# Kernel optimization log

Measured on AMD Instinct MI355X. Metric: run time of the kernel, lower is better.

The kernel has to match this reference:

```python
import jax, jax.numpy as jnp
import numpy as np

B, CIN, COUT, K, H, W = 16, 256, 256, 3, 64, 64
COND = 512


def setup_inputs() -> dict:
    key = jax.random.key(0)
    ks = jax.random.split(key, 10)
    X = jax.random.normal(ks[0], (B, CIN, H, W), dtype=jnp.float32)
    cond_v = jax.random.normal(ks[1], (B, COND), dtype=jnp.float32)
    # conv weight [O, I, kh, kw]
    conv_w = jax.random.normal(ks[2], (COUT, CIN, K, K), dtype=jnp.float32) / np.sqrt(CIN * K * K)
    w0 = jax.random.normal(ks[3], (COND, COND), dtype=jnp.float32) / np.sqrt(COND)
    b0 = jnp.zeros((COND,), dtype=jnp.float32)
    w1 = jax.random.normal(ks[4], (COND, COND), dtype=jnp.float32) / np.sqrt(COND)
    b1 = jnp.zeros((COND,), dtype=jnp.float32)
    w_out = jax.random.normal(ks[5], (CIN, COND), dtype=jnp.float32) / np.sqrt(COND)
    b_out = jnp.zeros((CIN,), dtype=jnp.float32)
    return {"X": X, "cond_v": cond_v, "conv_w": conv_w,
            "w0": w0, "b0": b0, "w1": w1, "b1": b1,
            "w_out": w_out, "b_out": b_out}


def reference(X, cond_v, conv_w, w0, b0, w1, b1, w_out, b_out):
    # proj_cond MLP: (Linear+SiLU) x depth, final Linear -> in_channels
    h = jax.nn.silu(cond_v @ w0.T + b0)
    h = jax.nn.silu(h @ w1.T + b1)
    scale = h @ w_out.T + b_out + 1.0          # [B, I]
    # modulate: bw[b,o,i,kh,kw] = w[o,i,kh,kw] * scale[b,i]
    bw = conv_w[None] * scale[:, None, :, None, None]
    # demodulate across (i, kh, kw)
    demod = jax.lax.rsqrt(jnp.sum(bw * bw, axis=(2, 3, 4)) + 1e-8)  # [B, O]
    bw = bw * demod[:, :, None, None, None]
    b, o, i, kh, kw = bw.shape
    # per-sample conv via grouped conv: x -> [1, B*I, H, W], w -> [B*O, I, kh, kw]
    x = X.reshape(1, b * i, X.shape[2], X.shape[3])
    w = bw.reshape(b * o, i, kh, kw)
    out = jax.lax.conv_general_dilated(
        x, w, window_strides=(1, 1), padding="SAME",
        feature_group_count=b,
        dimension_numbers=("NCHW", "OIHW", "NCHW"))
    return out.reshape(b, o, out.shape[2], out.shape[3])
```

## Files before the change

### kernel.cpp

```cpp
#include <hip/hip_runtime.h>
#include <hip/hip_bf16.h>
#include <cstdint>

#define NB 16
#define CI 256
#define CO 256
#define HH 64
#define WW 64
#define CC 512
#define HP 66
#define WP 66

typedef short short8 __attribute__((ext_vector_type(8)));
typedef float floatx4 __attribute__((ext_vector_type(4)));
typedef unsigned int uintx4 __attribute__((ext_vector_type(4)));

__device__ __forceinline__ void g2lds16(const void* g, void* l) {
  __builtin_amdgcn_global_load_lds((const __attribute__((address_space(1))) void*)g,
                                   (__attribute__((address_space(3))) void*)l, 16, 0, 0);
}

#define ASM_VMCNT0() do { asm volatile("s_waitcnt vmcnt(0)" ::: "memory"); \
                          __builtin_amdgcn_sched_barrier(0); } while (0)
#define ASM_VMCNT2() do { asm volatile("s_waitcnt vmcnt(2)" ::: "memory"); \
                          __builtin_amdgcn_sched_barrier(0); } while (0)
#define RAW_BAR() do { __builtin_amdgcn_sched_barrier(0);  \
                       __builtin_amdgcn_s_barrier();       \
                       __builtin_amdgcn_sched_barrier(0); } while (0)

__global__ void k_zero_halo(__hip_bfloat16* __restrict__ Xs) {
  int gid = blockIdx.x * 256 + threadIdx.x;
  int job = gid >> 5;
  int unit = gid & 31;
  int b = job / 260;
  int p = job % 260;
  if (b >= NB) return;
  int hp, wp;
  if (p < 66)       { hp = 0;       wp = p; }
  else if (p < 132) { hp = 65;      wp = p - 66; }
  else if (p < 196) { hp = p - 131; wp = 0; }
  else              { hp = p - 195; wp = 65; }
  uintx4 z = {0u, 0u, 0u, 0u};
  *reinterpret_cast<uintx4*>(Xs + ((((size_t)b * HP + hp) * WP + wp) * CI + unit * 8)) = z;
}

template<int KD, int N, bool SILU, bool PLUSONE, int BJ>
__global__ void k_mlp(const float* __restrict__ in, const float* __restrict__ w,
                      const float* __restrict__ bias, float* __restrict__ out) {
  __shared__ float4 sin4[KD / 4];
  const int nb = N / BJ;
  int b = blockIdx.x / nb;
  int j = (blockIdx.x % nb) * BJ + threadIdx.x;
  const float4* in4 = reinterpret_cast<const float4*>(in + (size_t)b * KD);
  for (int k = threadIdx.x; k < KD / 4; k += BJ) sin4[k] = in4[k];
  __syncthreads();
  float acc = bias[j];
  const float4* wr = reinterpret_cast<const float4*>(w + (size_t)j * KD);
#pragma unroll 8
  for (int kk = 0; kk < KD / 4; ++kk) {
    float4 wv = wr[kk];
    float4 sv = sin4[kk];
    acc += wv.x * sv.x + wv.y * sv.y + wv.z * sv.z + wv.w * sv.w;
  }
  if (SILU) acc = acc / (1.0f + __expf(-acc));
  if (PLUSONE) acc += 1.0f;
  out[(size_t)b * N + j] = acc;
}

__global__ void k_repack(const float* __restrict__ cw, __hip_bfloat16* __restrict__ Wt,
                         float* __restrict__ wsq) {
  int gid = blockIdx.x * 256 + threadIdx.x;
  if (gid >= CO * CI) return;
  const float* p = cw + (size_t)gid * 9;
  float s = 0.0f;
#pragma unroll
  for (int t = 0; t < 9; ++t) {
    float v = p[t];
    s += v * v;
    Wt[(size_t)t * CO * CI + gid] = __float2bfloat16(v);
  }
  wsq[gid] = s;
}

__global__ void k_demod(const float* __restrict__ wsq, const float* __restrict__ scale,
                        float* __restrict__ demod) {
  __shared__ float s2[CI];
  int b = blockIdx.x;
  int o = threadIdx.x;
  float sv = scale[b * CI + o];
  s2[o] = sv * sv;
  __syncthreads();
  float acc = 0.0f;
  const float4* wr = reinterpret_cast<const float4*>(wsq + (size_t)o * CI);
  const float4* s4 = reinterpret_cast<const float4*>(s2);
#pragma unroll 8
  for (int i = 0; i < CI / 4; ++i) {
    float4 wv = wr[i];
    float4 sq = s4[i];
    acc += wv.x * sq.x + wv.y * sq.y + wv.z * sq.z + wv.w * sq.w;
  }
  demod[b * CO + o] = rsqrtf(acc + 1e-8f);
}

__global__ void k_scalex(const float* __restrict__ X, const float* __restrict__ scale,
                         __hip_bfloat16* __restrict__ Xs) {
  __shared__ float tile[64][68];
  __shared__ float ssc[64];
  int bid = blockIdx.x;
  int b = bid >> 8;
  int rem = bid & 255;
  int h = rem >> 2;
  int i0 = (rem & 3) * 64;
  int t = threadIdx.x;
  if (t < 64) ssc[t] = scale[b * CI + i0 + t];
  const float* src = X + (((size_t)b * CI + i0) * HH + h) * WW;
  int ii_base = t >> 4;
  int w4 = (t & 15) * 4;
#pragma unroll
  for (int r2 = 0; r2 < 4; ++r2) {
    int ii = r2 * 16 + ii_base;
    *reinterpret_cast<float4*>(&tile[ii][w4]) =
        *reinterpret_cast<const float4*>(src + (size_t)ii * HH * WW + w4);
  }
  __syncthreads();
  int u = t & 7;
  int wl = t >> 3;
#pragma unroll
  for (int iter = 0; iter < 2; ++iter) {
    int w2 = wl + iter * 32;
    union { unsigned short us[8]; uintx4 v; } pk;
#pragma unroll
    for (int j = 0; j < 8; ++j) {
      int ii = u * 8 + j;
      float v = tile[ii][w2] * ssc[ii];
      __hip_bfloat16 hb = __float2bfloat16(v);
      pk.us[j] = *reinterpret_cast<unsigned short*>(&hb);
    }
    *reinterpret_cast<uintx4*>(Xs + ((((size_t)b * HP + (h + 1)) * WP + (w2 + 1)) * CI + i0 + u * 8)) = pk.v;
  }
}

__global__ __launch_bounds__(512, 4)
void k_conv(const __hip_bfloat16* __restrict__ Xs, const __hip_bfloat16* __restrict__ Wt,
            const float* __restrict__ demod, float* __restrict__ out) {
  __shared__ __align__(16) char lds[33792 + 2 * 16384];
  char* sX  = lds;
  char* sA0 = lds + 33792;

  int bid = blockIdx.x;
  int b = bid >> 6;
  int rem = bid & 63;
  int ht = rem >> 1;
  int ob = rem & 1;
  int h0 = ht * 2;
  int o0 = ob * 128;

  int tid = threadIdx.x;
  int wv = tid >> 6;
  int lane = tid & 63;
  int lhi = lane >> 4;
  int llo = lane & 15;
  int wo = wv >> 2;
  int wq = wv & 3;
  int r = wq >> 1;
  int c0 = (wq & 1) * 32;

  floatx4 acc[4][2];
#pragma unroll
  for (int m = 0; m < 4; ++m)
#pragma unroll
    for (int n = 0; n < 2; ++n) acc[m][n] = (floatx4){0.f, 0.f, 0.f, 0.f};

  int row_a[4], ra7[4];
#pragma unroll
  for (int m = 0; m < 4; ++m) { row_a[m] = wo * 64 + m * 16 + llo; ra7[m] = row_a[m] & 7; }

  const __hip_bfloat16* xs_img = Xs + (size_t)b * HP * WP * CI;

  for (int ic = 0; ic < 4; ++ic) {
    for (int j = wv; j < 33; j += 8) {
      int u = j * 64 + lane;
      int row = u >> 3;
      int slot = lane & 7;
      int lr = row / 66;
      int wp = row - lr * 66;
      int isel = ic * 64 + ((slot ^ (row & 7)) << 3);
      const __hip_bfloat16* src = xs_img + (((size_t)(h0 + lr) * WP + wp) * CI + isel);
      g2lds16(src, sX + j * 1024);
    }
    {
      const __hip_bfloat16* wbase = Wt + (size_t)o0 * CI + ic * 64;
#pragma unroll
      for (int jj = 0; jj < 2; ++jj) {
        int j = wv + jj * 8;
        int row = j * 8 + (lane >> 3);
        int slot = lane & 7;
        int isel = (slot ^ (row & 7)) << 3;
        g2lds16(wbase + (size_t)row * CI + isel, sA0 + j * 1024);
      }
    }
    ASM_VMCNT0();
    RAW_BAR();

    for (int t = 0; t < 9; ++t) {
      char* sA = sA0 + (t & 1) * 16384;
      if (t < 8) {
        const __hip_bfloat16* wbase = Wt + (size_t)(t + 1) * CO * CI + (size_t)o0 * CI + ic * 64;
        char* dst = sA0 + ((t + 1) & 1) * 16384;
#pragma unroll
        for (int jj = 0; jj < 2; ++jj) {
          int j = wv + jj * 8;
          int row = j * 8 + (lane >> 3);
          int slot = lane & 7;
          int isel = (slot ^ (row & 7)) << 3;
          g2lds16(wbase + (size_t)row * CI + isel, dst + j * 1024);
        }
        ASM_VMCNT2();
      } else {
        ASM_VMCNT0();
      }
      RAW_BAR();

      int kh = t / 3;
      int kw = t - kh * 3;
#pragma unroll
      for (int k32 = 0; k32 < 2; ++k32) {
        short8 af[4], bq[2];
#pragma unroll
        for (int m = 0; m < 4; ++m) {
          int addr = row_a[m] * 128 + (((k32 * 4 + lhi) ^ ra7[m]) << 4);
          af[m] = *reinterpret_cast<const short8*>(sA + addr);
        }
#pragma unroll
        for (int n = 0; n < 2; ++n) {
          int tr = (r + kh) * 66 + c0 + n * 16 + llo + kw;
          int addr = tr * 128 + (((k32 * 4 + lhi) ^ (tr & 7)) << 4);
          bq[n] = *reinterpret_cast<const short8*>(sX + addr);
        }
#pragma unroll
        for (int m = 0; m < 4; ++m)
#pragma unroll
          for (int n = 0; n < 2; ++n)
            acc[m][n] = __builtin_amdgcn_mfma_f32_16x16x32_bf16(af[m], bq[n], acc[m][n], 0, 0, 0);
      }
      RAW_BAR();
    }
  }

  const float* dmrow = demod + b * CO + o0 + wo * 64;
  float* obase = out + (((size_t)b * CO + o0 + wo * 64) * HH + (h0 + r)) * WW;
#pragma unroll
  for (int m = 0; m < 4; ++m) {
#pragma unroll
    for (int j = 0; j < 4; ++j) {
      int o_off = m * 16 + lhi * 4 + j;
      float dm = dmrow[o_off];
#pragma unroll
      for (int n = 0; n < 2; ++n) {
        int w = c0 + n * 16 + llo;
        obase[(size_t)o_off * HH * WW + w] = acc[m][n][j] * dm;
      }
    }
  }
}

extern "C" void kernel_launch(void* const* d_in, const int* in_sizes, int n_in,
                              void* d_out, int out_size, void* d_ws, size_t ws_size,
                              hipStream_t stream) {
  const float* X      = (const float*)d_in[0];
  const float* cond_v = (const float*)d_in[1];
  const float* conv_w = (const float*)d_in[2];
  const float* w0     = (const float*)d_in[3];
  const float* b0     = (const float*)d_in[4];
  const float* w1     = (const float*)d_in[5];
  const float* b1     = (const float*)d_in[6];
  const float* w_out  = (const float*)d_in[7];
  const float* b_out  = (const float*)d_in[8];
  float* out = (float*)d_out;

  char* ws = (char*)d_ws;
  const size_t XS_BYTES  = (size_t)NB * HP * WP * CI * 2;
  const size_t WT_BYTES  = (size_t)9 * CO * CI * 2;
  const size_t WSQ_BYTES = (size_t)CO * CI * 4;
  __hip_bfloat16* Xs = (__hip_bfloat16*)ws;
  __hip_bfloat16* Wt = (__hip_bfloat16*)(ws + XS_BYTES);
  float* wsq   = (float*)(ws + XS_BYTES + WT_BYTES);
  float* h0b   = (float*)(ws + XS_BYTES + WT_BYTES + WSQ_BYTES);
  float* h1b   = h0b + NB * CC;
  float* scale = h1b + NB * CC;
  float* demod = scale + NB * CI;

  k_zero_halo<<<520, 256, 0, stream>>>(Xs);
  k_repack<<<(CO * CI) / 256, 256, 0, stream>>>(conv_w, Wt, wsq);
  k_mlp<CC, CC, true, false, 128><<<NB * (CC / 128), 128, 0, stream>>>(cond_v, w0, b0, h0b);
  k_mlp<CC, CC, true, false, 128><<<NB * (CC / 128), 128, 0, stream>>>(h0b, w1, b1, h1b);
  k_mlp<CC, CI, false, true, 128><<<NB * (CI / 128), 128, 0, stream>>>(h1b, w_out, b_out, scale);
  k_demod<<<NB, CO, 0, stream>>>(wsq, scale, demod);
  k_scalex<<<NB * 64 * 4, 256, 0, stream>>>(X, scale, Xs);
  k_conv<<<NB * 32 * 2, 512, 0, stream>>>(Xs, Wt, demod, out);
}
```

Before: 139.2 us.

## Enlarge conv tile to all output channels, fuse halo zeroing, swizzle transpose tile

The conv kernel now gives each workgroup all 256 output channels and 4 output rows, so the input halo tile is loaded once per workgroup instead of twice. Each wave accumulates 4x8 MFMA tiles, and a remapped block index spreads work across XCDs. Halo zeroing moves into the scale/transpose kernel, removing one launch, and that kernel's LDS transpose tile gets an XOR swizzle to cut bank conflicts. The trade-off is far higher LDS and register use per block (occupancy bound drops from 4 to 2) and only 256 workgroups in the grid, which may underfill the GPU.

```diff
diff --git a/kernel.cpp b/kernel.cpp
--- a/kernel.cpp
+++ b/kernel.cpp
@@ -22,27 +22,11 @@
 
 #define ASM_VMCNT0() do { asm volatile("s_waitcnt vmcnt(0)" ::: "memory"); \
                           __builtin_amdgcn_sched_barrier(0); } while (0)
-#define ASM_VMCNT2() do { asm volatile("s_waitcnt vmcnt(2)" ::: "memory"); \
+#define ASM_VMCNT4() do { asm volatile("s_waitcnt vmcnt(4)" ::: "memory"); \
                           __builtin_amdgcn_sched_barrier(0); } while (0)
 #define RAW_BAR() do { __builtin_amdgcn_sched_barrier(0);  \
                        __builtin_amdgcn_s_barrier();       \
                        __builtin_amdgcn_sched_barrier(0); } while (0)
-
-__global__ void k_zero_halo(__hip_bfloat16* __restrict__ Xs) {
-  int gid = blockIdx.x * 256 + threadIdx.x;
-  int job = gid >> 5;
-  int unit = gid & 31;
-  int b = job / 260;
-  int p = job % 260;
-  if (b >= NB) return;
-  int hp, wp;
-  if (p < 66)       { hp = 0;       wp = p; }
-  else if (p < 132) { hp = 65;      wp = p - 66; }
-  else if (p < 196) { hp = p - 131; wp = 0; }
-  else              { hp = p - 195; wp = 65; }
-  uintx4 z = {0u, 0u, 0u, 0u};
-  *reinterpret_cast<uintx4*>(Xs + ((((size_t)b * HP + hp) * WP + wp) * CI + unit * 8)) = z;
-}
 
 template<int KD, int N, bool SILU, bool PLUSONE, int BJ>
 __global__ void k_mlp(const float* __restrict__ in, const float* __restrict__ w,
@@ -113,18 +97,41 @@
   int i0 = (rem & 3) * 64;
   int t = threadIdx.x;
   if (t < 64) ssc[t] = scale[b * CI + i0 + t];
+
+  __hip_bfloat16* xs_img = Xs + (size_t)b * HP * WP * CI;
+  uintx4 z = {0u, 0u, 0u, 0u};
+  if (t < 16) {
+    int px = (t >> 3) * 65;
+    int sl = t & 7;
+    *reinterpret_cast<uintx4*>(xs_img + (((size_t)(h + 1)) * WP + px) * CI + i0 + sl * 8) = z;
+  }
+  if (h == 0) {
+    for (int u = t; u < 66 * 8; u += 256) {
+      int px = u >> 3, sl = u & 7;
+      *reinterpret_cast<uintx4*>(xs_img + ((size_t)px) * CI + i0 + sl * 8) = z;
+    }
+  }
+  if (h == 63) {
+    for (int u = t; u < 66 * 8; u += 256) {
+      int px = u >> 3, sl = u & 7;
+      *reinterpret_cast<uintx4*>(xs_img + ((size_t)65 * WP + px) * CI + i0 + sl * 8) = z;
+    }
+  }
+
   const float* src = X + (((size_t)b * CI + i0) * HH + h) * WW;
   int ii_base = t >> 4;
   int w4 = (t & 15) * 4;
 #pragma unroll
   for (int r2 = 0; r2 < 4; ++r2) {
     int ii = r2 * 16 + ii_base;
-    *reinterpret_cast<float4*>(&tile[ii][w4]) =
+    int key = ((ii >> 3) & 7) << 2;
+    *reinterpret_cast<float4*>(&tile[ii][w4 ^ key]) =
         *reinterpret_cast<const float4*>(src + (size_t)ii * HH * WW + w4);
   }
   __syncthreads();
   int u = t & 7;
   int wl = t >> 3;
+  int key = u << 2;
 #pragma unroll
   for (int iter = 0; iter < 2; ++iter) {
     int w2 = wl + iter * 32;
@@ -132,44 +139,39 @@
 #pragma unroll
     for (int j = 0; j < 8; ++j) {
       int ii = u * 8 + j;
-      float v = tile[ii][w2] * ssc[ii];
+      float v = tile[ii][w2 ^ key] * ssc[ii];
       __hip_bfloat16 hb = __float2bfloat16(v);
       pk.us[j] = *reinterpret_cast<unsigned short*>(&hb);
     }
-    *reinterpret_cast<uintx4*>(Xs + ((((size_t)b * HP + (h + 1)) * WP + (w2 + 1)) * CI + i0 + u * 8)) = pk.v;
-  }
-}
-
-__global__ __launch_bounds__(512, 4)
+    *reinterpret_cast<uintx4*>(xs_img + (((size_t)(h + 1)) * WP + (w2 + 1)) * CI + i0 + u * 8) = pk.v;
+  }
+}
+
+__global__ __launch_bounds__(512, 2)
 void k_conv(const __hip_bfloat16* __restrict__ Xs, const __hip_bfloat16* __restrict__ Wt,
             const float* __restrict__ demod, float* __restrict__ out) {
-  __shared__ __align__(16) char lds[33792 + 2 * 16384];
+  __shared__ __align__(16) char lds[55296 + 2 * 32768];
   char* sX  = lds;
-  char* sA0 = lds + 33792;
-
-  int bid = blockIdx.x;
-  int b = bid >> 6;
-  int rem = bid & 63;
-  int ht = rem >> 1;
-  int ob = rem & 1;
-  int h0 = ht * 2;
-  int o0 = ob * 128;
+  char* sA0 = lds + 55296;
+
+  int wg = (blockIdx.x & 7) * 32 + (blockIdx.x >> 3);
+  int b = wg >> 4;
+  int ht = wg & 15;
+  int h0 = ht * 4;
 
   int tid = threadIdx.x;
   int wv = tid >> 6;
   int lane = tid & 63;
   int lhi = lane >> 4;
   int llo = lane & 15;
-  int wo = wv >> 2;
-  int wq = wv & 3;
-  int r = wq >> 1;
-  int c0 = (wq & 1) * 32;
-
-  floatx4 acc[4][2];
+  int wo = wv >> 1;
+  int wpx = wv & 1;
+
+  floatx4 acc[4][8];
 #pragma unroll
   for (int m = 0; m < 4; ++m)
 #pragma unroll
-    for (int n = 0; n < 2; ++n) acc[m][n] = (floatx4){0.f, 0.f, 0.f, 0.f};
+    for (int n = 0; n < 8; ++n) acc[m][n] = (floatx4){0.f, 0.f, 0.f, 0.f};
 
   int row_a[4], ra7[4];
 #pragma unroll
@@ -178,21 +180,22 @@
   const __hip_bfloat16* xs_img = Xs + (size_t)b * HP * WP * CI;
 
   for (int ic = 0; ic < 4; ++ic) {
-    for (int j = wv; j < 33; j += 8) {
+    for (int j = wv; j < 54; j += 8) {
       int u = j * 64 + lane;
-      int row = u >> 3;
+      int pr = u >> 3;
       int slot = lane & 7;
-      int lr = row / 66;
-      int wp = row - lr * 66;
-      int isel = ic * 64 + ((slot ^ (row & 7)) << 3);
+      int lr = pr / 72;
+      int wp = pr - lr * 72;
+      if (wp > 65) wp = 65;
+      int isel = ic * 64 + ((slot ^ (pr & 7)) << 3);
       const __hip_bfloat16* src = xs_img + (((size_t)(h0 + lr) * WP + wp) * CI + isel);
       g2lds16(src, sX + j * 1024);
     }
     {
-      const __hip_bfloat16* wbase = Wt + (size_t)o0 * CI + ic * 64;
-#pragma unroll
-      for (int jj = 0; jj < 2; ++jj) {
-        int j = wv + jj * 8;
+      const __hip_bfloat16* wbase = Wt + ic * 64;
+#pragma unroll
+      for (int jj = 0; jj < 4; ++jj) {
+        int j = wv * 4 + jj;
         int row = j * 8 + (lane >> 3);
         int slot = lane & 7;
         int isel = (slot ^ (row & 7)) << 3;
@@ -203,19 +206,19 @@
     RAW_BAR();
 
     for (int t = 0; t < 9; ++t) {
-      char* sA = sA0 + (t & 1) * 16384;
+      char* sA = sA0 + (t & 1) * 32768;
       if (t < 8) {
-        const __hip_bfloat16* wbase = Wt + (size_t)(t + 1) * CO * CI + (size_t)o0 * CI + ic * 64;
-        char* dst = sA0 + ((t + 1) & 1) * 16384;
-#pragma unroll
-        for (int jj = 0; jj < 2; ++jj) {
-          int j = wv + jj * 8;
+        const __hip_bfloat16* wbase = Wt + (size_t)(t + 1) * CO * CI + ic * 64;
+        char* dst = sA0 + ((t + 1) & 1) * 32768;
+#pragma unroll
+        for (int jj = 0; jj < 4; ++jj) {
+          int j = wv * 4 + jj;
           int row = j * 8 + (lane >> 3);
           int slot = lane & 7;
           int isel = (slot ^ (row & 7)) << 3;
           g2lds16(wbase + (size_t)row * CI + isel, dst + j * 1024);
         }
-        ASM_VMCNT2();
+        ASM_VMCNT4();
       } else {
         ASM_VMCNT0();
       }
@@ -225,40 +228,43 @@
       int kw = t - kh * 3;
 #pragma unroll
       for (int k32 = 0; k32 < 2; ++k32) {
-        short8 af[4], bq[2];
+        int kidx = k32 * 4 + lhi;
+        short8 af[4];
 #pragma unroll
         for (int m = 0; m < 4; ++m) {
-          int addr = row_a[m] * 128 + (((k32 * 4 + lhi) ^ ra7[m]) << 4);
+          int addr = row_a[m] * 128 + ((kidx ^ ra7[m]) << 4);
           af[m] = *reinterpret_cast<const short8*>(sA + addr);
         }
 #pragma unroll
-        for (int n = 0; n < 2; ++n) {
-          int tr = (r + kh) * 66 + c0 + n * 16 + llo + kw;
-          int addr = tr * 128 + (((k32 * 4 + lhi) ^ (tr & 7)) << 4);
-          bq[n] = *reinterpret_cast<const short8*>(sX + addr);
+        for (int n = 0; n < 8; ++n) {
+          int stripe = wpx * 2 + (n >> 2) + kh;
+          int px = (n & 3) * 16 + llo + kw;
+          int prl = stripe * 72 + px;
+          int addr = prl * 128 + ((kidx ^ (prl & 7)) << 4);
+          short8 bq = *reinterpret_cast<const short8*>(sX + addr);
+#pragma unroll
+          for (int m = 0; m < 4; ++m)
+            acc[m][n] = __builtin_amdgcn_mfma_f32_16x16x32_bf16(af[m], bq, acc[m][n], 0, 0, 0);
         }
-#pragma unroll
-        for (int m = 0; m < 4; ++m)
-#pragma unroll
-          for (int n = 0; n < 2; ++n)
-            acc[m][n] = __builtin_amdgcn_mfma_f32_16x16x32_bf16(af[m], bq[n], acc[m][n], 0, 0, 0);
       }
       RAW_BAR();
     }
   }
 
-  const float* dmrow = demod + b * CO + o0 + wo * 64;
-  float* obase = out + (((size_t)b * CO + o0 + wo * 64) * HH + (h0 + r)) * WW;
 #pragma unroll
   for (int m = 0; m < 4; ++m) {
+    int obase_o = wo * 64 + m * 16 + lhi * 4;
+    float4 dmv = *reinterpret_cast<const float4*>(demod + (size_t)b * CO + obase_o);
 #pragma unroll
     for (int j = 0; j < 4; ++j) {
-      int o_off = m * 16 + lhi * 4 + j;
-      float dm = dmrow[o_off];
-#pragma unroll
-      for (int n = 0; n < 2; ++n) {
-        int w = c0 + n * 16 + llo;
-        obase[(size_t)o_off * HH * WW + w] = acc[m][n][j] * dm;
+      int o = obase_o + j;
+      float dm = (j == 0) ? dmv.x : (j == 1) ? dmv.y : (j == 2) ? dmv.z : dmv.w;
+      float* orow = out + (((size_t)b * CO + o) * HH + h0) * WW;
+#pragma unroll
+      for (int n = 0; n < 8; ++n) {
+        int row = wpx * 2 + (n >> 2);
+        int col = (n & 3) * 16 + llo;
+        orow[(size_t)row * WW + col] = acc[m][n][j] * dm;
       }
     }
   }
@@ -290,12 +296,11 @@
   float* scale = h1b + NB * CC;
   float* demod = scale + NB * CI;
 
-  k_zero_halo<<<520, 256, 0, stream>>>(Xs);
   k_repack<<<(CO * CI) / 256, 256, 0, stream>>>(conv_w, Wt, wsq);
   k_mlp<CC, CC, true, false, 128><<<NB * (CC / 128), 128, 0, stream>>>(cond_v, w0, b0, h0b);
   k_mlp<CC, CC, true, false, 128><<<NB * (CC / 128), 128, 0, stream>>>(h0b, w1, b1, h1b);
   k_mlp<CC, CI, false, true, 128><<<NB * (CI / 128), 128, 0, stream>>>(h1b, w_out, b_out, scale);
   k_demod<<<NB, CO, 0, stream>>>(wsq, scale, demod);
   k_scalex<<<NB * 64 * 4, 256, 0, stream>>>(X, scale, Xs);
-  k_conv<<<NB * 32 * 2, 512, 0, stream>>>(Xs, Wt, demod, out);
-}
+  k_conv<<<NB * 16, 512, 0, stream>>>(Xs, Wt, demod, out);
+}
```

Result: faster. 135.9 us (-2.3%).
